# Kernel optimization log

Measured on AMD Instinct MI355X. Metric: run time of the kernel, lower is better.

The kernel has to match this reference:

```python
import jax, jax.numpy as jnp
import numpy as np

B, NQ, NKV = 2, 2048, 2048
DIM, CTX_DIM = 1024, 1024
HEADS, DIM_HEAD = 16, 64
INNER = HEADS * DIM_HEAD  # 1024
SCALE = DIM_HEAD ** -0.5


def setup_inputs() -> dict:
    key = jax.random.key(0)
    ks = jax.random.split(key, 6)
    x = jax.random.normal(ks[0], (B, NQ, DIM), dtype=jnp.float32)
    context = jax.random.normal(ks[1], (B, NKV, CTX_DIM), dtype=jnp.float32)
    # nn.Linear weights stored as [out, in] in torch; we keep [in, out] for x @ W.
    Wq = jax.random.normal(ks[2], (DIM, INNER), dtype=jnp.float32) / np.sqrt(DIM)
    Wkv = jax.random.normal(ks[3], (CTX_DIM, 2 * INNER), dtype=jnp.float32) / np.sqrt(CTX_DIM)
    Wout = jax.random.normal(ks[4], (INNER, DIM), dtype=jnp.float32) / np.sqrt(INNER)
    bout = jax.random.normal(ks[5], (DIM,), dtype=jnp.float32) * 0.01
    return {"x": x, "context": context, "Wq": Wq, "Wkv": Wkv, "Wout": Wout, "bout": bout}


def reference(x, context, Wq, Wkv, Wout, bout):
    q = x @ Wq                      # [B, Nq, inner]
    kv = context @ Wkv              # [B, Nkv, 2*inner]
    k, v = jnp.split(kv, 2, axis=-1)

    def split_heads(t):             # [B, N, inner] -> [B, H, N, dh]
        return t.reshape(t.shape[0], t.shape[1], HEADS, DIM_HEAD).transpose(0, 2, 1, 3)

    q, k, v = split_heads(q), split_heads(k), split_heads(v)
    dots = jnp.einsum('bhqd,bhkd->bhqk', q, k) * SCALE  # [B, H, Nq, Nkv]
    attn = jax.nn.softmax(dots, axis=-1)
    out = jnp.einsum('bhqk,bhkd->bhqd', attn, v)        # [B, H, Nq, dh]
    out = out.transpose(0, 2, 1, 3).reshape(out.shape[0], out.shape[2], INNER)
    return out @ Wout + bout        # [B, Nq, dim]
```

## Files before the change

### kernel.cpp

```cpp
#include <hip/hip_runtime.h>
#include <hip/hip_bf16.h>
#include <stdint.h>

#define NQ 2048
#define NKV 2048
#define DIM 1024
#define INNER 1024
#define HEADS 16
#define DH 64
#define BATCH 2

typedef float f32x4 __attribute__((ext_vector_type(4)));
typedef __bf16 bf16x8 __attribute__((ext_vector_type(8)));
typedef unsigned int u32x4 __attribute__((ext_vector_type(4)));

__device__ inline ushort f2b(float f) {
    uint32_t u = __builtin_bit_cast(uint32_t, f);
    u += 0x7fff + ((u >> 16) & 1);
    return (ushort)(u >> 16);
}

__device__ inline uint pkbf16(float lo, float hi) {
    __hip_bfloat162 h = __float22bfloat162_rn(make_float2(lo, hi));
    uint r;
    __builtin_memcpy(&r, &h, 4);
    return r;
}

__device__ __forceinline__ void gload16(const void* g, void* lds) {
    __builtin_amdgcn_global_load_lds(
        (const __attribute__((address_space(1))) unsigned int*)g,
        (__attribute__((address_space(3))) unsigned int*)lds, 16, 0, 0);
}

__global__ void prep(const float* __restrict__ x, const float* __restrict__ ctx,
                     const float* __restrict__ Wq, const float* __restrict__ Wkv,
                     const float* __restrict__ Wout,
                     ushort* __restrict__ xb, ushort* __restrict__ cb,
                     ushort* __restrict__ Wqt, ushort* __restrict__ Wkvt,
                     ushort* __restrict__ Woutt) {
    int z = blockIdx.z;
    if (z < 4) {
        __shared__ ushort tile[32][33];
        const float* src; ushort* dst; int C;
        if (z == 0)      { src = Wq;          dst = Wqt;                C = 1024; }
        else if (z == 1) { src = Wkv;         dst = Wkvt;               C = 2048; }
        else if (z == 2) { src = Wkv + 1024;  dst = Wkvt + 1024 * 1024; C = 2048; }
        else             { src = Wout;        dst = Woutt;              C = 1024; }
        int c0 = blockIdx.x * 32, r0 = blockIdx.y * 32;
        int tx = threadIdx.x, ty = threadIdx.y;
#pragma unroll
        for (int i = 0; i < 4; i++)
            tile[ty + i * 8][tx] = f2b(src[(size_t)(r0 + ty + i * 8) * C + c0 + tx]);
        __syncthreads();
#pragma unroll
        for (int i = 0; i < 4; i++)
            dst[(size_t)(c0 + ty + i * 8) * 1024 + r0 + tx] = tile[tx][ty + i * 8];
    } else {
        const int n4 = (BATCH * NQ * DIM) / 4;
        int fb = blockIdx.y * 32 + blockIdx.x;
        int t = threadIdx.y * 32 + threadIdx.x;
        for (int i = fb * 256 + t; i < 2 * n4; i += 1024 * 256) {
            float4 v;
            if (i < n4) v = ((const float4*)x)[i];
            else        v = ((const float4*)ctx)[i - n4];
            ushort4 o;
            o.x = f2b(v.x); o.y = f2b(v.y); o.z = f2b(v.z); o.w = f2b(v.w);
            if (i < n4) ((ushort4*)xb)[i] = o;
            else        ((ushort4*)cb)[i - n4] = o;
        }
    }
}

__global__ __launch_bounds__(256) void gemm_qkv(const ushort* __restrict__ xb, const ushort* __restrict__ cb,
                                                const ushort* __restrict__ Wqt, const ushort* __restrict__ Wkvt,
                                                ushort* __restrict__ qb, ushort* __restrict__ kb,
                                                ushort* __restrict__ vtb, float qscale) {
    constexpr int K = 1024;
    __shared__ ushort As[2][4096];
    __shared__ ushort Bs[2][4096];
    int bid = blockIdx.x;
    bool isq = bid < 256;
    const ushort *A, *Bt;
    int m0, n0;
    if (isq) { A = xb; Bt = Wqt;  m0 = (bid >> 3) * 128; n0 = (bid & 7) * 128; }
    else     { int b2 = bid - 256; A = cb; Bt = Wkvt; m0 = (b2 >> 4) * 128; n0 = (b2 & 15) * 128; }
    int t = threadIdx.x, l = t & 63, w = t >> 6;
    int wr = w >> 1, wc = w & 1;
    int lg = l >> 4, lc = l & 15;
    f32x4 acc[4][4] = {};

    auto stage = [&](int buf, int k0) {
#pragma unroll
        for (int i = 0; i < 2; i++) {
            int s = w + i * 4;
            gload16(A + (size_t)(m0 + (s & 1) * 64 + l) * K + k0 + (s >> 1) * 8, &As[buf][s * 512]);
            gload16(Bt + (size_t)(n0 + (s & 1) * 64 + l) * K + k0 + (s >> 1) * 8, &Bs[buf][s * 512]);
        }
    };

    stage(0, 0);
    for (int k0 = 0, tt = 0; k0 < K; k0 += 32, ++tt) {
        int cur = tt & 1;
        if (k0 + 32 < K) {
            stage(cur ^ 1, k0 + 32);
            asm volatile("s_waitcnt vmcnt(4)" ::: "memory");
        } else {
            asm volatile("s_waitcnt vmcnt(0)" ::: "memory");
        }
        __builtin_amdgcn_s_barrier();
        asm volatile("" ::: "memory");
        bf16x8 af[4], bf[4];
#pragma unroll
        for (int mi = 0; mi < 4; mi++)
            af[mi] = *(const bf16x8*)&As[cur][(lg * 128 + wr * 64 + mi * 16 + lc) * 8];
#pragma unroll
        for (int ni = 0; ni < 4; ni++)
            bf[ni] = *(const bf16x8*)&Bs[cur][(lg * 128 + wc * 64 + ni * 16 + lc) * 8];
        __builtin_amdgcn_s_setprio(1);
#pragma unroll
        for (int mi = 0; mi < 4; mi++)
#pragma unroll
            for (int ni = 0; ni < 4; ni++)
                acc[mi][ni] = __builtin_amdgcn_mfma_f32_16x16x32_bf16(af[mi], bf[ni], acc[mi][ni], 0, 0, 0);
        __builtin_amdgcn_s_setprio(0);
        asm volatile("s_waitcnt lgkmcnt(0)" ::: "memory");
        __builtin_amdgcn_s_barrier();
        asm volatile("" ::: "memory");
    }
    if (isq) {
#pragma unroll
        for (int mi = 0; mi < 4; mi++)
#pragma unroll
            for (int ni = 0; ni < 4; ni++)
#pragma unroll
                for (int r = 0; r < 4; r++) {
                    int m = m0 + wr * 64 + mi * 16 + lg * 4 + r;
                    int n = n0 + wc * 64 + ni * 16 + lc;
                    qb[(size_t)m * 1024 + n] = f2b(acc[mi][ni][r] * qscale);
                }
    } else if (n0 < 1024) {
#pragma unroll
        for (int mi = 0; mi < 4; mi++)
#pragma unroll
            for (int ni = 0; ni < 4; ni++)
#pragma unroll
                for (int r = 0; r < 4; r++) {
                    int m = m0 + wr * 64 + mi * 16 + lg * 4 + r;
                    int n = n0 + wc * 64 + ni * 16 + lc;
                    kb[(size_t)m * 1024 + n] = f2b(acc[mi][ni][r]);
                }
    } else {
#pragma unroll
        for (int mi = 0; mi < 4; mi++)
#pragma unroll
            for (int ni = 0; ni < 4; ni++) {
                int n = n0 - 1024 + wc * 64 + ni * 16 + lc;
                int h = n >> 6, d = n & 63;
                int mrow = m0 + wr * 64 + mi * 16 + lg * 4;
                int b = mrow >> 11, kv = mrow & 2047;
                ushort4 pk;
                pk.x = f2b(acc[mi][ni][0]); pk.y = f2b(acc[mi][ni][1]);
                pk.z = f2b(acc[mi][ni][2]); pk.w = f2b(acc[mi][ni][3]);
                *(ushort4*)&vtb[(((size_t)b * HEADS + h) * DH + d) * (size_t)NKV + kv] = pk;
            }
    }
}

__global__ __launch_bounds__(256) void gemm_out(const ushort* __restrict__ A, const ushort* __restrict__ Bt,
                                                float* __restrict__ C0, const float* __restrict__ bias,
                                                int M, int N, int K) {
    __shared__ ushort As[2][4096];
    __shared__ ushort Bs[2][2048];
    int m0 = blockIdx.y * 128, n0 = blockIdx.x * 64;
    int t = threadIdx.x, l = t & 63, w = t >> 6;
    int wr = w >> 1, wc = w & 1;
    int lg = l >> 4, lc = l & 15;
    f32x4 acc[4][2] = {};

    auto stage = [&](int buf, int k0) {
#pragma unroll
        for (int i = 0; i < 2; i++) {
            int s = w + i * 4;
            gload16(A + (size_t)(m0 + (s & 1) * 64 + l) * K + k0 + (s >> 1) * 8, &As[buf][s * 512]);
        }
        gload16(Bt + (size_t)(n0 + l) * K + k0 + w * 8, &Bs[buf][w * 512]);
    };

    stage(0, 0);
    for (int k0 = 0, tt = 0; k0 < K; k0 += 32, ++tt) {
        int cur = tt & 1;
        if (k0 + 32 < K) {
            stage(cur ^ 1, k0 + 32);
            asm volatile("s_waitcnt vmcnt(3)" ::: "memory");
        } else {
            asm volatile("s_waitcnt vmcnt(0)" ::: "memory");
        }
        __builtin_amdgcn_s_barrier();
        asm volatile("" ::: "memory");
        bf16x8 af[4], bf[2];
#pragma unroll
        for (int mi = 0; mi < 4; mi++)
            af[mi] = *(const bf16x8*)&As[cur][(lg * 128 + wr * 64 + mi * 16 + lc) * 8];
#pragma unroll
        for (int ni = 0; ni < 2; ni++)
            bf[ni] = *(const bf16x8*)&Bs[cur][(lg * 64 + wc * 32 + ni * 16 + lc) * 8];
        __builtin_amdgcn_s_setprio(1);
#pragma unroll
        for (int mi = 0; mi < 4; mi++)
#pragma unroll
            for (int ni = 0; ni < 2; ni++)
                acc[mi][ni] = __builtin_amdgcn_mfma_f32_16x16x32_bf16(af[mi], bf[ni], acc[mi][ni], 0, 0, 0);
        __builtin_amdgcn_s_setprio(0);
        asm volatile("s_waitcnt lgkmcnt(0)" ::: "memory");
        __builtin_amdgcn_s_barrier();
        asm volatile("" ::: "memory");
    }
#pragma unroll
    for (int mi = 0; mi < 4; mi++)
#pragma unroll
        for (int ni = 0; ni < 2; ni++)
#pragma unroll
            for (int r = 0; r < 4; r++) {
                int m = m0 + wr * 64 + mi * 16 + lg * 4 + r;
                int n = n0 + wc * 32 + ni * 16 + lc;
                C0[(size_t)m * N + n] = acc[mi][ni][r] + bias[n];
            }
}

__global__ __launch_bounds__(256, 3) void attn3(const ushort* __restrict__ qb, const ushort* __restrict__ kb,
                                                const ushort* __restrict__ vtb, ushort* __restrict__ ob) {
    __shared__ ushort Qs[8 * 128 * 8];
    __shared__ ushort Ks[2][4096];
    __shared__ ushort Vs[2][4096];
    int flat = blockIdx.x;
    int swz = (flat & 7) * 64 + (flat >> 3);
    int qt = swz & 15, h = (swz >> 4) & 15, b = swz >> 8;
    int t = threadIdx.x, l = t & 63, w = t >> 6;
    int lg = l >> 4, lc = l & 15;
    int xsw = (lc << 1) & 0x1C;
    const ushort* Qg = qb + (size_t)b * NQ * INNER + h * DH;
    const ushort* Kg = kb + (size_t)b * NKV * INNER + h * DH;
    const ushort* Vg = vtb + (((size_t)b * HEADS + h) * DH) * NKV;
    int q0 = qt * 128;

#pragma unroll
    for (int i = 0; i < 4; i++) {
        int s = w * 4 + i;
        gload16(Qg + (size_t)(q0 + (s & 1) * 64 + l) * INNER + (s >> 1) * 8, &Qs[s * 512]);
    }
    auto stageKV = [&](int buf, int kv0) {
#pragma unroll
        for (int i = 0; i < 2; i++) {
            int s = w + i * 4;
            gload16(Kg + (size_t)(kv0 + l) * INNER + s * 8, &Ks[buf][s * 512]);
            gload16(Vg + (size_t)l * NKV + kv0 + s * 8, &Vs[buf][s * 512]);
        }
    };
    stageKV(0, 0);
    __syncthreads();

    bf16x8 qf[2][2];
#pragma unroll
    for (int mi = 0; mi < 2; mi++)
#pragma unroll
        for (int kc = 0; kc < 2; kc++)
            qf[mi][kc] = *(const bf16x8*)&Qs[((kc * 4 + lg) * 128 + w * 32 + mi * 16 + lc) * 8];
    __syncthreads();

    uint* Ps = (uint*)Qs + w * 1024;
    f32x4 o[2][4] = {};
    float m_[2] = {-1e30f, -1e30f}, s_[2] = {0.f, 0.f};

    for (int tt = 0; tt < NKV / 64; ++tt) {
        int cur = tt & 1;
        if (tt + 1 < NKV / 64) stageKV(cur ^ 1, (tt + 1) * 64);
        f32x4 st[2][4] = {};
        __builtin_amdgcn_s_setprio(1);
#pragma unroll
        for (int kc = 0; kc < 2; kc++)
#pragma unroll
            for (int nb = 0; nb < 4; nb++) {
                bf16x8 kf = *(const bf16x8*)&Ks[cur][((kc * 4 + lg) * 64 + nb * 16 + lc) * 8];
                st[0][nb] = __builtin_amdgcn_mfma_f32_16x16x32_bf16(kf, qf[0][kc], st[0][nb], 0, 0, 0);
                st[1][nb] = __builtin_amdgcn_mfma_f32_16x16x32_bf16(kf, qf[1][kc], st[1][nb], 0, 0, 0);
            }
        __builtin_amdgcn_s_setprio(0);
#pragma unroll
        for (int mi = 0; mi < 2; mi++) {
            float mx = st[mi][0][0];
#pragma unroll
            for (int nb = 0; nb < 4; nb++)
#pragma unroll
                for (int r = 0; r < 4; r++) mx = fmaxf(mx, st[mi][nb][r]);
            mx = fmaxf(mx, __shfl_xor(mx, 16));
            mx = fmaxf(mx, __shfl_xor(mx, 32));
            if (!__all(mx - m_[mi] <= 8.f)) {
                float mn = fmaxf(m_[mi], mx);
                float fac = __builtin_amdgcn_exp2f(m_[mi] - mn);
                m_[mi] = mn;
                s_[mi] *= fac;
#pragma unroll
                for (int nb = 0; nb < 4; nb++) o[mi][nb] *= fac;
            }
            float mn = m_[mi];
            float rs = 0.f;
#pragma unroll
            for (int nb = 0; nb < 4; nb++) {
                float p0 = __builtin_amdgcn_exp2f(st[mi][nb][0] - mn);
                float p1 = __builtin_amdgcn_exp2f(st[mi][nb][1] - mn);
                float p2 = __builtin_amdgcn_exp2f(st[mi][nb][2] - mn);
                float p3 = __builtin_amdgcn_exp2f(st[mi][nb][3] - mn);
                rs += (p0 + p1) + (p2 + p3);
                uint2 pw;
                pw.x = pkbf16(p0, p1);
                pw.y = pkbf16(p2, p3);
                *(uint2*)&Ps[(mi * 16 + lc) * 32 + ((nb * 8 + lg * 2) ^ xsw)] = pw;
            }
            rs += __shfl_xor(rs, 16);
            rs += __shfl_xor(rs, 32);
            s_[mi] += rs;
        }
        asm volatile("" ::: "memory");
        bf16x8 pf[2][2], vf[4][2];
#pragma unroll
        for (int mi = 0; mi < 2; mi++)
#pragma unroll
            for (int kc = 0; kc < 2; kc++)
                pf[mi][kc] = *(const bf16x8*)&Ps[(mi * 16 + lc) * 32 + ((kc * 16 + lg * 4) ^ xsw)];
#pragma unroll
        for (int nb = 0; nb < 4; nb++)
#pragma unroll
            for (int kc = 0; kc < 2; kc++)
                vf[nb][kc] = *(const bf16x8*)&Vs[cur][((kc * 4 + lg) * 64 + nb * 16 + lc) * 8];
        __builtin_amdgcn_s_setprio(1);
#pragma unroll
        for (int nb = 0; nb < 4; nb++)
#pragma unroll
            for (int kc = 0; kc < 2; kc++) {
                o[0][nb] = __builtin_amdgcn_mfma_f32_16x16x32_bf16(vf[nb][kc], pf[0][kc], o[0][nb], 0, 0, 0);
                o[1][nb] = __builtin_amdgcn_mfma_f32_16x16x32_bf16(vf[nb][kc], pf[1][kc], o[1][nb], 0, 0, 0);
            }
        __builtin_amdgcn_s_setprio(0);
        __syncthreads();
    }
    ushort* Og = ob + (size_t)b * NQ * INNER + h * DH;
#pragma unroll
    for (int mi = 0; mi < 2; mi++) {
        float inv = 1.f / s_[mi];
        int q = q0 + w * 32 + mi * 16 + lc;
#pragma unroll
        for (int nb = 0; nb < 4; nb++) {
            uint2 pw;
            pw.x = pkbf16(o[mi][nb][0] * inv, o[mi][nb][1] * inv);
            pw.y = pkbf16(o[mi][nb][2] * inv, o[mi][nb][3] * inv);
            *(uint2*)&Og[(size_t)q * INNER + nb * 16 + lg * 4] = pw;
        }
    }
}

extern "C" void kernel_launch(void* const* d_in, const int* in_sizes, int n_in,
                              void* d_out, int out_size, void* d_ws, size_t ws_size,
                              hipStream_t stream) {
    const float* x    = (const float*)d_in[0];
    const float* ctx  = (const float*)d_in[1];
    const float* Wq   = (const float*)d_in[2];
    const float* Wkv  = (const float*)d_in[3];
    const float* Wout = (const float*)d_in[4];
    const float* bout = (const float*)d_in[5];
    float* out = (float*)d_out;

    if (ws_size < (size_t)(56u << 20)) return;
    char* ws = (char*)d_ws;
    ushort* xb    = (ushort*)(ws);
    ushort* cb    = (ushort*)(ws + (8u << 20));
    ushort* ob    = (ushort*)(ws + (8u << 20));
    ushort* qb    = (ushort*)(ws + (16u << 20));
    ushort* kb    = (ushort*)(ws + (24u << 20));
    ushort* vtb   = (ushort*)(ws + (32u << 20));
    ushort* Wqt   = (ushort*)(ws + (48u << 20));
    ushort* Wkvt  = (ushort*)(ws + (50u << 20));
    ushort* Woutt = (ushort*)(ws + (54u << 20));

    prep<<<dim3(32, 32, 5), dim3(32, 8), 0, stream>>>(x, ctx, Wq, Wkv, Wout, xb, cb, Wqt, Wkvt, Woutt);
    gemm_qkv<<<768, 256, 0, stream>>>(xb, cb, Wqt, Wkvt, qb, kb, vtb, 0.125f * 1.44269504f);
    attn3<<<512, 256, 0, stream>>>(qb, kb, vtb, ob);
    gemm_out<<<dim3(16, 32), 256, 0, stream>>>(ob, Woutt, out, bout, 4096, 1024, 1024);
}
```

Measured before the change: 193.1 us.

## Shrink QKV GEMM tiles, swizzle block order, and stage V transpose through LDS

The QKV projection GEMM tile drops from 128x128 to 128x64, doubling the grid to 1536 blocks so more CUs are busy. Block indices are remapped with an XCD-aware swizzle in both projection GEMMs, which should improve L2 locality across the chiplets. The transposed V store now goes through shared memory, so each thread writes 16-byte contiguous rows instead of scattered 8-byte pieces. In exchange, the smaller tiles reuse each loaded A row less and add an extra barrier in the V epilogue.

```diff
diff --git a/kernel.cpp b/kernel.cpp
--- a/kernel.cpp
+++ b/kernel.cpp
@@ -77,26 +77,26 @@
                                                 ushort* __restrict__ qb, ushort* __restrict__ kb,
                                                 ushort* __restrict__ vtb, float qscale) {
     constexpr int K = 1024;
-    __shared__ ushort As[2][4096];
-    __shared__ ushort Bs[2][4096];
-    int bid = blockIdx.x;
-    bool isq = bid < 256;
+    __shared__ ushort lds[12288];
+    int flat = blockIdx.x;
+    int swz = (flat & 7) * 192 + (flat >> 3);
+    bool isq = swz < 512;
     const ushort *A, *Bt;
     int m0, n0;
-    if (isq) { A = xb; Bt = Wqt;  m0 = (bid >> 3) * 128; n0 = (bid & 7) * 128; }
-    else     { int b2 = bid - 256; A = cb; Bt = Wkvt; m0 = (b2 >> 4) * 128; n0 = (b2 & 15) * 128; }
+    if (isq) { A = xb; Bt = Wqt;  m0 = (swz >> 4) * 128;  n0 = (swz & 15) * 64; }
+    else     { int b2 = swz - 512; A = cb; Bt = Wkvt; m0 = (b2 >> 5) * 128; n0 = (b2 & 31) * 64; }
     int t = threadIdx.x, l = t & 63, w = t >> 6;
     int wr = w >> 1, wc = w & 1;
     int lg = l >> 4, lc = l & 15;
-    f32x4 acc[4][4] = {};
+    f32x4 acc[4][2] = {};
 
     auto stage = [&](int buf, int k0) {
 #pragma unroll
         for (int i = 0; i < 2; i++) {
             int s = w + i * 4;
-            gload16(A + (size_t)(m0 + (s & 1) * 64 + l) * K + k0 + (s >> 1) * 8, &As[buf][s * 512]);
-            gload16(Bt + (size_t)(n0 + (s & 1) * 64 + l) * K + k0 + (s >> 1) * 8, &Bs[buf][s * 512]);
-        }
+            gload16(A + (size_t)(m0 + (s & 1) * 64 + l) * K + k0 + (s >> 1) * 8, &lds[buf * 4096 + s * 512]);
+        }
+        gload16(Bt + (size_t)(n0 + l) * K + k0 + w * 8, &lds[8192 + buf * 2048 + w * 512]);
     };
 
     stage(0, 0);
@@ -104,24 +104,24 @@
         int cur = tt & 1;
         if (k0 + 32 < K) {
             stage(cur ^ 1, k0 + 32);
-            asm volatile("s_waitcnt vmcnt(4)" ::: "memory");
+            asm volatile("s_waitcnt vmcnt(3)" ::: "memory");
         } else {
             asm volatile("s_waitcnt vmcnt(0)" ::: "memory");
         }
         __builtin_amdgcn_s_barrier();
         asm volatile("" ::: "memory");
-        bf16x8 af[4], bf[4];
-#pragma unroll
-        for (int mi = 0; mi < 4; mi++)
-            af[mi] = *(const bf16x8*)&As[cur][(lg * 128 + wr * 64 + mi * 16 + lc) * 8];
-#pragma unroll
-        for (int ni = 0; ni < 4; ni++)
-            bf[ni] = *(const bf16x8*)&Bs[cur][(lg * 128 + wc * 64 + ni * 16 + lc) * 8];
+        bf16x8 af[4], bf[2];
+#pragma unroll
+        for (int mi = 0; mi < 4; mi++)
+            af[mi] = *(const bf16x8*)&lds[cur * 4096 + (lg * 128 + wr * 64 + mi * 16 + lc) * 8];
+#pragma unroll
+        for (int ni = 0; ni < 2; ni++)
+            bf[ni] = *(const bf16x8*)&lds[8192 + cur * 2048 + (lg * 64 + wc * 32 + ni * 16 + lc) * 8];
         __builtin_amdgcn_s_setprio(1);
 #pragma unroll
         for (int mi = 0; mi < 4; mi++)
 #pragma unroll
-            for (int ni = 0; ni < 4; ni++)
+            for (int ni = 0; ni < 2; ni++)
                 acc[mi][ni] = __builtin_amdgcn_mfma_f32_16x16x32_bf16(af[mi], bf[ni], acc[mi][ni], 0, 0, 0);
         __builtin_amdgcn_s_setprio(0);
         asm volatile("s_waitcnt lgkmcnt(0)" ::: "memory");
@@ -132,38 +132,44 @@
 #pragma unroll
         for (int mi = 0; mi < 4; mi++)
 #pragma unroll
-            for (int ni = 0; ni < 4; ni++)
+            for (int ni = 0; ni < 2; ni++)
 #pragma unroll
                 for (int r = 0; r < 4; r++) {
                     int m = m0 + wr * 64 + mi * 16 + lg * 4 + r;
-                    int n = n0 + wc * 64 + ni * 16 + lc;
+                    int n = n0 + wc * 32 + ni * 16 + lc;
                     qb[(size_t)m * 1024 + n] = f2b(acc[mi][ni][r] * qscale);
                 }
     } else if (n0 < 1024) {
 #pragma unroll
         for (int mi = 0; mi < 4; mi++)
 #pragma unroll
-            for (int ni = 0; ni < 4; ni++)
+            for (int ni = 0; ni < 2; ni++)
 #pragma unroll
                 for (int r = 0; r < 4; r++) {
                     int m = m0 + wr * 64 + mi * 16 + lg * 4 + r;
-                    int n = n0 + wc * 64 + ni * 16 + lc;
+                    int n = n0 + wc * 32 + ni * 16 + lc;
                     kb[(size_t)m * 1024 + n] = f2b(acc[mi][ni][r]);
                 }
     } else {
-#pragma unroll
-        for (int mi = 0; mi < 4; mi++)
-#pragma unroll
-            for (int ni = 0; ni < 4; ni++) {
-                int n = n0 - 1024 + wc * 64 + ni * 16 + lc;
-                int h = n >> 6, d = n & 63;
-                int mrow = m0 + wr * 64 + mi * 16 + lg * 4;
-                int b = mrow >> 11, kv = mrow & 2047;
-                ushort4 pk;
-                pk.x = f2b(acc[mi][ni][0]); pk.y = f2b(acc[mi][ni][1]);
-                pk.z = f2b(acc[mi][ni][2]); pk.w = f2b(acc[mi][ni][3]);
-                *(ushort4*)&vtb[(((size_t)b * HEADS + h) * DH + d) * (size_t)NKV + kv] = pk;
-            }
+        int b = m0 >> 11, kv0 = m0 & 2047;
+        int h = (n0 - 1024) >> 6;
+#pragma unroll
+        for (int mi = 0; mi < 4; mi++)
+#pragma unroll
+            for (int ni = 0; ni < 2; ni++)
+#pragma unroll
+                for (int r = 0; r < 4; r++) {
+                    int ml = wr * 64 + mi * 16 + lg * 4 + r;
+                    int nl = wc * 32 + ni * 16 + lc;
+                    lds[nl * 136 + ml] = f2b(acc[mi][ni][r]);
+                }
+        __syncthreads();
+#pragma unroll
+        for (int c = 0; c < 4; c++) {
+            int d = t >> 2, chunk = (t & 3) + c * 4;
+            u32x4 v = *(u32x4*)&lds[d * 136 + chunk * 8];
+            *(u32x4*)&vtb[(((size_t)b * HEADS + h) * DH + d) * (size_t)NKV + kv0 + chunk * 8] = v;
+        }
     }
 }
 
@@ -172,7 +178,9 @@
                                                 int M, int N, int K) {
     __shared__ ushort As[2][4096];
     __shared__ ushort Bs[2][2048];
-    int m0 = blockIdx.y * 128, n0 = blockIdx.x * 64;
+    int flat = blockIdx.x;
+    int swz = (flat & 7) * 64 + (flat >> 3);
+    int m0 = (swz >> 4) * 128, n0 = (swz & 15) * 64;
     int t = threadIdx.x, l = t & 63, w = t >> 6;
     int wr = w >> 1, wc = w & 1;
     int lg = l >> 4, lc = l & 15;
@@ -383,7 +391,7 @@
     ushort* Woutt = (ushort*)(ws + (54u << 20));
 
     prep<<<dim3(32, 32, 5), dim3(32, 8), 0, stream>>>(x, ctx, Wq, Wkv, Wout, xb, cb, Wqt, Wkvt, Woutt);
-    gemm_qkv<<<768, 256, 0, stream>>>(xb, cb, Wqt, Wkvt, qb, kb, vtb, 0.125f * 1.44269504f);
+    gemm_qkv<<<1536, 256, 0, stream>>>(xb, cb, Wqt, Wkvt, qb, kb, vtb, 0.125f * 1.44269504f);
     attn3<<<512, 256, 0, stream>>>(qb, kb, vtb, ob);
-    gemm_out<<<dim3(16, 32), 256, 0, stream>>>(ob, Woutt, out, bout, 4096, 1024, 1024);
-}
+    gemm_out<<<512, 256, 0, stream>>>(ob, Woutt, out, bout, 4096, 1024, 1024);
+}
```

After: 193.0 us. No clear change (-0.0%).

## Triple-buffer GEMM loads, swizzle block order, stage V-transpose via LDS, widen out tiles

Applied to the files above, without the earlier changes.

Both GEMM kernels move from double to triple buffering in one shared LDS array, keeping two tiles in flight with adjusted vmcnt waits. Block indices are swizzled so that consecutive blocks share operand tiles in cache. The V-transpose epilogue now goes through LDS so global stores are 16-byte contiguous along the kv dimension instead of scattered 8-byte stores. The output GEMM switches from 128x64 to 128x128 tiles with 256 blocks. The changes add LDS use and register pressure, and leave fewer blocks in the out GEMM.

```diff
diff --git a/kernel.cpp b/kernel.cpp
--- a/kernel.cpp
+++ b/kernel.cpp
@@ -76,15 +76,15 @@
                                                 const ushort* __restrict__ Wqt, const ushort* __restrict__ Wkvt,
                                                 ushort* __restrict__ qb, ushort* __restrict__ kb,
                                                 ushort* __restrict__ vtb, float qscale) {
-    constexpr int K = 1024;
-    __shared__ ushort As[2][4096];
-    __shared__ ushort Bs[2][4096];
-    int bid = blockIdx.x;
-    bool isq = bid < 256;
+    constexpr int K = 1024, NT = 32;
+    __shared__ ushort lds[24576];
+    int flat = blockIdx.x;
+    int swz = (flat & 7) * 96 + (flat >> 3);
+    bool isq = swz < 256;
     const ushort *A, *Bt;
     int m0, n0;
-    if (isq) { A = xb; Bt = Wqt;  m0 = (bid >> 3) * 128; n0 = (bid & 7) * 128; }
-    else     { int b2 = bid - 256; A = cb; Bt = Wkvt; m0 = (b2 >> 4) * 128; n0 = (b2 & 15) * 128; }
+    if (isq) { A = xb; Bt = Wqt;  m0 = (swz >> 3) * 128;  n0 = (swz & 7) * 128; }
+    else     { int b2 = swz - 256; A = cb; Bt = Wkvt; m0 = (b2 >> 4) * 128; n0 = (b2 & 15) * 128; }
     int t = threadIdx.x, l = t & 63, w = t >> 6;
     int wr = w >> 1, wc = w & 1;
     int lg = l >> 4, lc = l & 15;
@@ -94,16 +94,19 @@
 #pragma unroll
         for (int i = 0; i < 2; i++) {
             int s = w + i * 4;
-            gload16(A + (size_t)(m0 + (s & 1) * 64 + l) * K + k0 + (s >> 1) * 8, &As[buf][s * 512]);
-            gload16(Bt + (size_t)(n0 + (s & 1) * 64 + l) * K + k0 + (s >> 1) * 8, &Bs[buf][s * 512]);
+            gload16(A + (size_t)(m0 + (s & 1) * 64 + l) * K + k0 + (s >> 1) * 8, &lds[buf * 8192 + s * 512]);
+            gload16(Bt + (size_t)(n0 + (s & 1) * 64 + l) * K + k0 + (s >> 1) * 8, &lds[buf * 8192 + 4096 + s * 512]);
         }
     };
 
     stage(0, 0);
-    for (int k0 = 0, tt = 0; k0 < K; k0 += 32, ++tt) {
-        int cur = tt & 1;
-        if (k0 + 32 < K) {
-            stage(cur ^ 1, k0 + 32);
+    stage(1, 32);
+    for (int tt = 0; tt < NT; ++tt) {
+        int cur = tt % 3;
+        if (tt + 2 < NT) {
+            stage((tt + 2) % 3, (tt + 2) * 32);
+            asm volatile("s_waitcnt vmcnt(8)" ::: "memory");
+        } else if (tt + 1 < NT) {
             asm volatile("s_waitcnt vmcnt(4)" ::: "memory");
         } else {
             asm volatile("s_waitcnt vmcnt(0)" ::: "memory");
@@ -113,10 +116,10 @@
         bf16x8 af[4], bf[4];
 #pragma unroll
         for (int mi = 0; mi < 4; mi++)
-            af[mi] = *(const bf16x8*)&As[cur][(lg * 128 + wr * 64 + mi * 16 + lc) * 8];
+            af[mi] = *(const bf16x8*)&lds[cur * 8192 + (lg * 128 + wr * 64 + mi * 16 + lc) * 8];
 #pragma unroll
         for (int ni = 0; ni < 4; ni++)
-            bf[ni] = *(const bf16x8*)&Bs[cur][(lg * 128 + wc * 64 + ni * 16 + lc) * 8];
+            bf[ni] = *(const bf16x8*)&lds[cur * 8192 + 4096 + (lg * 128 + wc * 64 + ni * 16 + lc) * 8];
         __builtin_amdgcn_s_setprio(1);
 #pragma unroll
         for (int mi = 0; mi < 4; mi++)
@@ -151,65 +154,78 @@
                     kb[(size_t)m * 1024 + n] = f2b(acc[mi][ni][r]);
                 }
     } else {
-#pragma unroll
-        for (int mi = 0; mi < 4; mi++)
-#pragma unroll
-            for (int ni = 0; ni < 4; ni++) {
-                int n = n0 - 1024 + wc * 64 + ni * 16 + lc;
-                int h = n >> 6, d = n & 63;
-                int mrow = m0 + wr * 64 + mi * 16 + lg * 4;
-                int b = mrow >> 11, kv = mrow & 2047;
-                ushort4 pk;
-                pk.x = f2b(acc[mi][ni][0]); pk.y = f2b(acc[mi][ni][1]);
-                pk.z = f2b(acc[mi][ni][2]); pk.w = f2b(acc[mi][ni][3]);
-                *(ushort4*)&vtb[(((size_t)b * HEADS + h) * DH + d) * (size_t)NKV + kv] = pk;
-            }
+        int b = m0 >> 11, kv0 = m0 & 2047;
+        int h0 = (n0 - 1024) >> 6;
+#pragma unroll
+        for (int mi = 0; mi < 4; mi++)
+#pragma unroll
+            for (int ni = 0; ni < 4; ni++)
+#pragma unroll
+                for (int r = 0; r < 4; r++) {
+                    int ml = wr * 64 + mi * 16 + lg * 4 + r;
+                    int nl = wc * 64 + ni * 16 + lc;
+                    lds[nl * 136 + ml] = f2b(acc[mi][ni][r]);
+                }
+        __syncthreads();
+#pragma unroll
+        for (int c = 0; c < 8; c++) {
+            int idx = c * 256 + t;
+            int rrow = idx >> 4;
+            int chunk = idx & 15;
+            int h = h0 + (rrow >> 6), d = rrow & 63;
+            u32x4 v = *(u32x4*)&lds[rrow * 136 + chunk * 8];
+            *(u32x4*)&vtb[(((size_t)b * HEADS + h) * DH + d) * (size_t)NKV + kv0 + chunk * 8] = v;
+        }
     }
 }
 
 __global__ __launch_bounds__(256) void gemm_out(const ushort* __restrict__ A, const ushort* __restrict__ Bt,
-                                                float* __restrict__ C0, const float* __restrict__ bias,
-                                                int M, int N, int K) {
-    __shared__ ushort As[2][4096];
-    __shared__ ushort Bs[2][2048];
-    int m0 = blockIdx.y * 128, n0 = blockIdx.x * 64;
+                                                float* __restrict__ C0, const float* __restrict__ bias) {
+    constexpr int K = 1024, NT = 32;
+    __shared__ ushort lds[24576];
+    int flat = blockIdx.x;
+    int swz = (flat & 7) * 32 + (flat >> 3);
+    int m0 = (swz >> 3) * 128, n0 = (swz & 7) * 128;
     int t = threadIdx.x, l = t & 63, w = t >> 6;
     int wr = w >> 1, wc = w & 1;
     int lg = l >> 4, lc = l & 15;
-    f32x4 acc[4][2] = {};
+    f32x4 acc[4][4] = {};
 
     auto stage = [&](int buf, int k0) {
 #pragma unroll
         for (int i = 0; i < 2; i++) {
             int s = w + i * 4;
-            gload16(A + (size_t)(m0 + (s & 1) * 64 + l) * K + k0 + (s >> 1) * 8, &As[buf][s * 512]);
-        }
-        gload16(Bt + (size_t)(n0 + l) * K + k0 + w * 8, &Bs[buf][w * 512]);
+            gload16(A + (size_t)(m0 + (s & 1) * 64 + l) * K + k0 + (s >> 1) * 8, &lds[buf * 8192 + s * 512]);
+            gload16(Bt + (size_t)(n0 + (s & 1) * 64 + l) * K + k0 + (s >> 1) * 8, &lds[buf * 8192 + 4096 + s * 512]);
+        }
     };
 
     stage(0, 0);
-    for (int k0 = 0, tt = 0; k0 < K; k0 += 32, ++tt) {
-        int cur = tt & 1;
-        if (k0 + 32 < K) {
-            stage(cur ^ 1, k0 + 32);
-            asm volatile("s_waitcnt vmcnt(3)" ::: "memory");
+    stage(1, 32);
+    for (int tt = 0; tt < NT; ++tt) {
+        int cur = tt % 3;
+        if (tt + 2 < NT) {
+            stage((tt + 2) % 3, (tt + 2) * 32);
+            asm volatile("s_waitcnt vmcnt(8)" ::: "memory");
+        } else if (tt + 1 < NT) {
+            asm volatile("s_waitcnt vmcnt(4)" ::: "memory");
         } else {
             asm volatile("s_waitcnt vmcnt(0)" ::: "memory");
         }
         __builtin_amdgcn_s_barrier();
         asm volatile("" ::: "memory");
-        bf16x8 af[4], bf[2];
-#pragma unroll
-        for (int mi = 0; mi < 4; mi++)
-            af[mi] = *(const bf16x8*)&As[cur][(lg * 128 + wr * 64 + mi * 16 + lc) * 8];
-#pragma unroll
-        for (int ni = 0; ni < 2; ni++)
-            bf[ni] = *(const bf16x8*)&Bs[cur][(lg * 64 + wc * 32 + ni * 16 + lc) * 8];
+        bf16x8 af[4], bf[4];
+#pragma unroll
+        for (int mi = 0; mi < 4; mi++)
+            af[mi] = *(const bf16x8*)&lds[cur * 8192 + (lg * 128 + wr * 64 + mi * 16 + lc) * 8];
+#pragma unroll
+        for (int ni = 0; ni < 4; ni++)
+            bf[ni] = *(const bf16x8*)&lds[cur * 8192 + 4096 + (lg * 128 + wc * 64 + ni * 16 + lc) * 8];
         __builtin_amdgcn_s_setprio(1);
 #pragma unroll
         for (int mi = 0; mi < 4; mi++)
 #pragma unroll
-            for (int ni = 0; ni < 2; ni++)
+            for (int ni = 0; ni < 4; ni++)
                 acc[mi][ni] = __builtin_amdgcn_mfma_f32_16x16x32_bf16(af[mi], bf[ni], acc[mi][ni], 0, 0, 0);
         __builtin_amdgcn_s_setprio(0);
         asm volatile("s_waitcnt lgkmcnt(0)" ::: "memory");
@@ -219,12 +235,12 @@
 #pragma unroll
     for (int mi = 0; mi < 4; mi++)
 #pragma unroll
-        for (int ni = 0; ni < 2; ni++)
+        for (int ni = 0; ni < 4; ni++)
 #pragma unroll
             for (int r = 0; r < 4; r++) {
                 int m = m0 + wr * 64 + mi * 16 + lg * 4 + r;
-                int n = n0 + wc * 32 + ni * 16 + lc;
-                C0[(size_t)m * N + n] = acc[mi][ni][r] + bias[n];
+                int n = n0 + wc * 64 + ni * 16 + lc;
+                C0[(size_t)m * 1024 + n] = acc[mi][ni][r] + bias[n];
             }
 }
 
@@ -385,5 +401,5 @@
     prep<<<dim3(32, 32, 5), dim3(32, 8), 0, stream>>>(x, ctx, Wq, Wkv, Wout, xb, cb, Wqt, Wkvt, Woutt);
     gemm_qkv<<<768, 256, 0, stream>>>(xb, cb, Wqt, Wkvt, qb, kb, vtb, 0.125f * 1.44269504f);
     attn3<<<512, 256, 0, stream>>>(qb, kb, vtb, ob);
-    gemm_out<<<dim3(16, 32), 256, 0, stream>>>(ob, Woutt, out, bout, 4096, 1024, 1024);
-}
+    gemm_out<<<256, 256, 0, stream>>>(ob, Woutt, out, bout);
+}
```

Measured after the change: 166.0 us. 1.16x faster.
